# Kernel optimization log

Measured on AMD Instinct MI355X. Metric: run time of the kernel, lower is better.

Reference implementation:

```python
import jax, jax.numpy as jnp
import numpy as np

B, I, H, MS, M = 8192, 1024, 1024, 64, 16
TAU = 1.0


def setup_inputs() -> dict:
    key = jax.random.key(0)
    ks = jax.random.split(key, 24)
    s = 0.02
    eps = 1e-6
    return {
        "x": jax.random.normal(ks[0], (B, I), jnp.float32),
        "h": jax.random.normal(ks[1], (B, H), jnp.float32),
        "c": jax.random.normal(ks[2], (B, H), jnp.float32),
        "memory": jax.random.normal(ks[3], (B, M, MS), jnp.float32),
        "u_gs": jax.random.uniform(ks[4], (B, M), jnp.float32, eps, 1.0 - eps),
        "u_a": jax.random.uniform(ks[5], (B, 1), jnp.float32, eps, 1.0 - eps),
        "u_b": jax.random.uniform(ks[6], (B, 1), jnp.float32, eps, 1.0 - eps),
        # pre-concatenated gate weights, matching torch.cat((W_x2*, W_h2*, W_c2*), 0)
        "W_i": jax.random.normal(ks[7], (I + 2 * H, H), jnp.float32) * s,
        "b_i": jnp.zeros((H,), jnp.float32),
        "W_f": jax.random.normal(ks[8], (I + 2 * H, H), jnp.float32) * s,
        "b_f": jnp.ones((H,), jnp.float32),
        "W_o": jax.random.normal(ks[9], (I + 2 * H, H), jnp.float32) * s,
        "b_o": jnp.zeros((H,), jnp.float32),
        "W_cand": jax.random.normal(ks[10], (I + H, H), jnp.float32) * s,
        "b_cand": jnp.zeros((H,), jnp.float32),
        "W_m": jax.random.normal(ks[11], (H, MS), jnp.float32) * s,
        "b_m": jnp.zeros((MS,), jnp.float32),
        "w_a_h": jax.random.normal(ks[12], (H, 1), jnp.float32) * s,
        "w_a_x": jax.random.normal(ks[13], (I, 1), jnp.float32) * s,
        "w_a_r": jax.random.normal(ks[14], (MS, 1), jnp.float32) * s,
        "w_b_h": jax.random.normal(ks[15], (H, 1), jnp.float32) * s,
        "w_b_x": jax.random.normal(ks[16], (I, 1), jnp.float32) * s,
        "w_b_r": jax.random.normal(ks[17], (MS, 1), jnp.float32) * s,
    }


def reference(x, h, c, memory, u_gs, u_a, u_b,
              W_i, b_i, W_f, b_f, W_o, b_o, W_cand, b_cand,
              W_m, b_m, w_a_h, w_a_x, w_a_r, w_b_h, w_b_x, w_b_r):
    # LSTM-style gates with peephole c in the concatenated input
    xhc = jnp.concatenate([x, h, c], axis=1)            # [B, I+2H]
    i = jax.nn.sigmoid(xhc @ W_i + b_i)
    f = jax.nn.sigmoid(xhc @ W_f + b_f)
    cp = jnp.tanh(jnp.concatenate([x, h], axis=1) @ W_cand + b_cand)
    c_new = f * c + i * cp
    o = jax.nn.sigmoid(jnp.concatenate([x, h, c_new], axis=1) @ W_o + b_o)
    h_new = o * jnp.tanh(c_new)

    # memory-slot attention with Gumbel-softmax sampling
    micro = h_new @ W_m + b_m                           # [B, MS]
    logits = jnp.einsum('bmk,bk->bm', memory, micro)    # [B, M]
    g = -jnp.log(-jnp.log(u_gs))                        # Gumbel(0,1)
    attn = jax.nn.softmax((logits + g) / TAU, axis=-1)  # sampled_locations
    sampled = jnp.einsum('bmk,bm->bk', memory, attn) + 1.0  # [B, MS]

    # gumbel-sigmoid (binary concrete) for alpha / beta
    la = jnp.log(u_a) - jnp.log1p(-u_a)
    lb = jnp.log(u_b) - jnp.log1p(-u_b)
    alpha = jax.nn.sigmoid((h_new @ w_a_h + x @ w_a_x + sampled @ w_a_r + la) / TAU)
    beta = jax.nn.sigmoid((h_new @ w_b_h + x @ w_b_x + sampled @ w_b_r + lb) / TAU)

    # [B, 2H+2]
    return jnp.concatenate([h_new, c_new, alpha, beta], axis=1)
```

## Files before the change

kernel.cpp:

```cpp
#include <hip/hip_runtime.h>

typedef __bf16 bfrag __attribute__((ext_vector_type(8)));
typedef float f32x4 __attribute__((ext_vector_type(4)));

#define GLDS16(g, l) __builtin_amdgcn_global_load_lds( \
    (__attribute__((address_space(1))) void*)(g),      \
    (__attribute__((address_space(3))) void*)(l), 16, 0, 0)

__device__ __forceinline__ float bf2f(ushort u) {
    return __uint_as_float(((unsigned)u) << 16);
}
__device__ __forceinline__ ushort f2bf(float f) {
    unsigned u = __float_as_uint(f);
    u += 0x7fff + ((u >> 16) & 1);
    return (ushort)(u >> 16);
}
__device__ __forceinline__ float sigmoidf_(float v) {
    return 1.0f / (1.0f + expf(-v));
}

__global__ __launch_bounds__(256) void k_castcat(const float* __restrict__ x,
                                                 const float* __restrict__ h,
                                                 const float* __restrict__ c,
                                                 ushort* __restrict__ xhcb) {
    int idx = blockIdx.x * 256 + threadIdx.x;
    int row = idx / 384;
    int c8 = (idx - row * 384) * 8;
    const float* s = (c8 < 1024) ? &x[(size_t)row * 1024 + c8]
                   : (c8 < 2048) ? &h[(size_t)row * 1024 + (c8 - 1024)]
                                 : &c[(size_t)row * 1024 + (c8 - 2048)];
    float4 a = *(const float4*)s;
    float4 b = *(const float4*)(s + 4);
    ushort tmp[8] = {f2bf(a.x), f2bf(a.y), f2bf(a.z), f2bf(a.w),
                     f2bf(b.x), f2bf(b.y), f2bf(b.z), f2bf(b.w)};
    *(uint4*)&xhcb[(size_t)idx * 8] = *(uint4*)tmp;
}

struct TD { const float* src; ushort* dst; int src_ld; int dst_ld; int ktiles; int off; };
struct TA { TD d[6]; };

__global__ __launch_bounds__(256) void k_transAll(TA a) {
    __shared__ float tile[64][65];
    int bid = blockIdx.x;
    int ri = 0;
#pragma unroll
    for (int i = 1; i < 6; ++i) ri = (bid >= a.d[i].off) ? i : ri;
    const float* src = a.d[ri].src;
    ushort* dst = a.d[ri].dst;
    int src_ld = a.d[ri].src_ld, dst_ld = a.d[ri].dst_ld;
    int local = bid - a.d[ri].off;
    int bx = local % a.d[ri].ktiles;
    int by = local / a.d[ri].ktiles;
    int k0 = bx * 64, n0 = by * 64;
    int t = threadIdx.x;
    int c4 = (t & 15) * 4;
    int r = t >> 4;
#pragma unroll
    for (int i = 0; i < 4; ++i) {
        int rr = r + i * 16;
        float4 v = *(const float4*)&src[(size_t)(k0 + rr) * src_ld + n0 + c4];
        tile[rr][c4 + 0] = v.x; tile[rr][c4 + 1] = v.y;
        tile[rr][c4 + 2] = v.z; tile[rr][c4 + 3] = v.w;
    }
    __syncthreads();
    int kk8 = (t & 7) * 8;
    int nn = t >> 3;
#pragma unroll
    for (int i = 0; i < 2; ++i) {
        int n = nn + i * 32;
        ushort tmp[8];
#pragma unroll
        for (int j = 0; j < 8; ++j) tmp[j] = f2bf(tile[kk8 + j][n]);
        *(uint4*)&dst[(size_t)(n0 + n) * dst_ld + k0 + kk8] = *(uint4*)tmp;
    }
}

__global__ void k_biasf(const float* bi, const float* bf_, const float* bc,
                        const float* bo, float* dst) {
    int t = blockIdx.x * 256 + threadIdx.x;
    int g = t >> 10, n = t & 1023;
    const float* s = (g == 0) ? bi : (g == 1) ? bf_ : (g == 2) ? bc : bo;
    dst[t] = s[n];
}

__global__ __launch_bounds__(256) void k_gemm1(const ushort* __restrict__ xhcb,
                                               const ushort* __restrict__ WT,
                                               const float* __restrict__ bias,
                                               ushort* __restrict__ Pre) {
    __shared__ __align__(16) ushort As[128 * 32];
    __shared__ __align__(16) ushort Bs[128 * 32];
    int t = threadIdx.x;
    int m0 = blockIdx.x * 128, n0 = blockIdx.y * 128;
    int Kext = (n0 >= 2048) ? 2048 : 3072;
    int w = t >> 6, l = t & 63;
    int wm = (w & 1) * 64, wn = (w >> 1) * 64;
    int lane16 = l & 15, quad = l >> 4;
    int sr = t >> 2;
    int sko = (((t & 3) ^ ((sr >> 1) & 3))) * 8;
    int sw8 = ((lane16 >> 1) & 3) * 8;
    f32x4 acc[4][4] = {};

    for (int k0 = 0; k0 < Kext; k0 += 32) {
        GLDS16(xhcb + (size_t)(m0 + sr) * 3072 + k0 + sko,       As + t * 8);
        GLDS16(xhcb + (size_t)(m0 + sr + 64) * 3072 + k0 + sko,  As + 2048 + t * 8);
        GLDS16(WT + (size_t)(n0 + sr) * 3072 + k0 + sko,         Bs + t * 8);
        GLDS16(WT + (size_t)(n0 + sr + 64) * 3072 + k0 + sko,    Bs + 2048 + t * 8);
        __syncthreads();
        bfrag af[4], bfr[4];
#pragma unroll
        for (int i = 0; i < 4; ++i) {
            af[i]  = *(const bfrag*)&As[(wm + i * 16 + lane16) * 32 + ((quad * 8) ^ sw8)];
            bfr[i] = *(const bfrag*)&Bs[(wn + i * 16 + lane16) * 32 + ((quad * 8) ^ sw8)];
        }
#pragma unroll
        for (int i = 0; i < 4; ++i)
#pragma unroll
            for (int j = 0; j < 4; ++j)
                acc[i][j] = __builtin_amdgcn_mfma_f32_16x16x32_bf16(af[i], bfr[j], acc[i][j], 0, 0, 0);
        __syncthreads();
    }
#pragma unroll
    for (int i = 0; i < 4; ++i) {
#pragma unroll
        for (int j = 0; j < 4; ++j) {
            int col = n0 + wn + j * 16 + lane16;
            float bv = bias[col];
            int rbase = m0 + wm + i * 16 + quad * 4;
#pragma unroll
            for (int r = 0; r < 4; ++r)
                Pre[(size_t)(rbase + r) * 4096 + col] = f2bf(acc[i][j][r] + bv);
        }
    }
}

__global__ __launch_bounds__(256) void k_cnew(const ushort* __restrict__ Pre,
                                              const float* __restrict__ cin,
                                              ushort* __restrict__ Cnewb,
                                              float* __restrict__ out) {
    int idx8 = blockIdx.x * 256 + threadIdx.x;
    int b = idx8 >> 7;
    int n8 = (idx8 & 127) * 8;
    uint4 vi = *(const uint4*)(Pre + (size_t)b * 4096 + n8);
    uint4 vf = *(const uint4*)(Pre + (size_t)b * 4096 + 1024 + n8);
    uint4 vc = *(const uint4*)(Pre + (size_t)b * 4096 + 2048 + n8);
    float4 c0 = *(const float4*)(cin + (size_t)b * 1024 + n8);
    float4 c1 = *(const float4*)(cin + (size_t)b * 1024 + n8 + 4);
    const ushort* pi = (const ushort*)&vi;
    const ushort* pf = (const ushort*)&vf;
    const ushort* pc = (const ushort*)&vc;
    float cv[8] = {c0.x, c0.y, c0.z, c0.w, c1.x, c1.y, c1.z, c1.w};
    float cn[8];
    ushort cb[8];
#pragma unroll
    for (int j = 0; j < 8; ++j) {
        float iv = sigmoidf_(bf2f(pi[j]));
        float fv = sigmoidf_(bf2f(pf[j]));
        float cp = tanhf(bf2f(pc[j]));
        cn[j] = fv * cv[j] + iv * cp;
        cb[j] = f2bf(cn[j]);
    }
    *(uint4*)(Cnewb + (size_t)b * 1024 + n8) = *(uint4*)cb;
    float* orow = out + (size_t)b * 2050 + 1024 + n8;
#pragma unroll
    for (int j = 0; j < 4; ++j)
        *(float2*)(orow + j * 2) = make_float2(cn[j * 2], cn[j * 2 + 1]);
}

__global__ __launch_bounds__(256) void k_gemm2(const ushort* __restrict__ Cnewb,
                                               const ushort* __restrict__ WoCT,
                                               const ushort* __restrict__ Pre,
                                               ushort* __restrict__ Hnewb,
                                               float* __restrict__ out) {
    __shared__ __align__(16) ushort As[128 * 32];
    __shared__ __align__(16) ushort Bs[128 * 32];
    int t = threadIdx.x;
    int m0 = blockIdx.x * 128, n0 = blockIdx.y * 128;
    int w = t >> 6, l = t & 63;
    int wm = (w & 1) * 64, wn = (w >> 1) * 64;
    int lane16 = l & 15, quad = l >> 4;
    int sr = t >> 2;
    int sko = (((t & 3) ^ ((sr >> 1) & 3))) * 8;
    int sw8 = ((lane16 >> 1) & 3) * 8;
    f32x4 acc[4][4] = {};

    for (int k0 = 0; k0 < 1024; k0 += 32) {
        GLDS16(Cnewb + (size_t)(m0 + sr) * 1024 + k0 + sko,       As + t * 8);
        GLDS16(Cnewb + (size_t)(m0 + sr + 64) * 1024 + k0 + sko,  As + 2048 + t * 8);
        GLDS16(WoCT + (size_t)(n0 + sr) * 1024 + k0 + sko,        Bs + t * 8);
        GLDS16(WoCT + (size_t)(n0 + sr + 64) * 1024 + k0 + sko,   Bs + 2048 + t * 8);
        __syncthreads();
        bfrag af[4], bfr[4];
#pragma unroll
        for (int i = 0; i < 4; ++i) {
            af[i]  = *(const bfrag*)&As[(wm + i * 16 + lane16) * 32 + ((quad * 8) ^ sw8)];
            bfr[i] = *(const bfrag*)&Bs[(wn + i * 16 + lane16) * 32 + ((quad * 8) ^ sw8)];
        }
#pragma unroll
        for (int i = 0; i < 4; ++i)
#pragma unroll
            for (int j = 0; j < 4; ++j)
                acc[i][j] = __builtin_amdgcn_mfma_f32_16x16x32_bf16(af[i], bfr[j], acc[i][j], 0, 0, 0);
        __syncthreads();
    }
#pragma unroll
    for (int i = 0; i < 4; ++i) {
#pragma unroll
        for (int j = 0; j < 4; ++j) {
            int col = n0 + wn + j * 16 + lane16;
            int rbase = m0 + wm + i * 16 + quad * 4;
#pragma unroll
            for (int r = 0; r < 4; ++r) {
                int row = rbase + r;
                float opre = acc[i][j][r] + bf2f(Pre[(size_t)row * 4096 + 3072 + col]);
                float o = sigmoidf_(opre);
                float cnv = bf2f(Cnewb[(size_t)row * 1024 + col]);
                float hv = o * tanhf(cnv);
                Hnewb[(size_t)row * 1024 + col] = f2bf(hv);
                out[(size_t)row * 2050 + col] = hv;
            }
        }
    }
}

__global__ __launch_bounds__(256) void k_attn(
    const ushort* __restrict__ Hnewb, const float* __restrict__ outr,
    const float* __restrict__ x, const float* __restrict__ memory,
    const float* __restrict__ u_gs, const float* __restrict__ u_a,
    const float* __restrict__ u_b, const ushort* __restrict__ WmT,
    const float* __restrict__ b_m,
    const float* __restrict__ w_a_h, const float* __restrict__ w_a_x,
    const float* __restrict__ w_a_r, const float* __restrict__ w_b_h,
    const float* __restrict__ w_b_x, const float* __restrict__ w_b_r,
    float* __restrict__ out) {
    __shared__ float sMicro[16 * 64];
    __shared__ float sAttn[16 * 16];
    __shared__ float sSamp[16 * 64];

    int b0 = blockIdx.x * 16;
    int t = threadIdx.x;
    int w = t >> 6, l = t & 63;
    int lane16 = l & 15, quad = l >> 4;

    {
        f32x4 acc = {0.f, 0.f, 0.f, 0.f};
        const ushort* Ab = Hnewb + (size_t)(b0 + lane16) * 1024 + quad * 8;
        const ushort* Bb = WmT + (size_t)(w * 16 + lane16) * 1024 + quad * 8;
#pragma unroll 4
        for (int k0 = 0; k0 < 1024; k0 += 32) {
            bfrag av = *(const bfrag*)(Ab + k0);
            bfrag bv = *(const bfrag*)(Bb + k0);
            acc = __builtin_amdgcn_mfma_f32_16x16x32_bf16(av, bv, acc, 0, 0, 0);
        }
        float bm = b_m[w * 16 + lane16];
#pragma unroll
        for (int r = 0; r < 4; ++r)
            sMicro[(quad * 4 + r) * 64 + w * 16 + lane16] = acc[r] + bm;
    }
    __syncthreads();

    {
        int r = t >> 4, m = t & 15;
        const float4* mem4 = (const float4*)(memory + (size_t)(b0 + r) * 1024 + m * 64);
        float lg = 0.f;
#pragma unroll
        for (int k4 = 0; k4 < 16; ++k4) {
            float4 mv = mem4[k4];
            const float* sm = &sMicro[r * 64 + k4 * 4];
            lg += mv.x * sm[0] + mv.y * sm[1] + mv.z * sm[2] + mv.w * sm[3];
        }
        float u = u_gs[(b0 + r) * 16 + m];
        float z = lg - logf(-logf(u));
        float zm = z;
        for (int off = 8; off; off >>= 1) zm = fmaxf(zm, __shfl_xor(zm, off, 16));
        float p = expf(z - zm);
        float ps = p;
        for (int off = 8; off; off >>= 1) ps += __shfl_xor(ps, off, 16);
        sAttn[r * 16 + m] = p / ps;
    }
    __syncthreads();

#pragma unroll
    for (int q = 0; q < 4; ++q) {
        int r = w * 4 + q;
        const float* mem = memory + (size_t)(b0 + r) * 1024 + l;
        float s = 0.f;
#pragma unroll
        for (int m = 0; m < 16; ++m) s += sAttn[r * 16 + m] * mem[m * 64];
        sSamp[r * 64 + l] = s + 1.0f;
    }
    __syncthreads();

    {
        int r = t >> 4, s16 = t & 15;
        size_t hoff = (size_t)(b0 + r) * 2050;
        size_t xoff = (size_t)(b0 + r) * 1024;
        float za = 0.f, zb = 0.f;
        for (int kk = 0; kk < 64; ++kk) {
            int k = s16 + kk * 16;
            float hv = outr[hoff + k];
            float xv = x[xoff + k];
            za += hv * w_a_h[k] + xv * w_a_x[k];
            zb += hv * w_b_h[k] + xv * w_b_x[k];
        }
#pragma unroll
        for (int k = s16 * 4; k < s16 * 4 + 4; ++k) {
            float sv = sSamp[r * 64 + k];
            za += sv * w_a_r[k];
            zb += sv * w_b_r[k];
        }
        for (int off = 8; off; off >>= 1) {
            za += __shfl_xor(za, off, 16);
            zb += __shfl_xor(zb, off, 16);
        }
        if (s16 == 0) {
            float ua = u_a[b0 + r];
            float ub = u_b[b0 + r];
            float la = logf(ua) - log1pf(-ua);
            float lb = logf(ub) - log1pf(-ub);
            out[(size_t)(b0 + r) * 2050 + 2048] = sigmoidf_(za + la);
            out[(size_t)(b0 + r) * 2050 + 2049] = sigmoidf_(zb + lb);
        }
    }
}

extern "C" void kernel_launch(void* const* d_in, const int* in_sizes, int n_in,
                              void* d_out, int out_size, void* d_ws, size_t ws_size,
                              hipStream_t stream) {
    const float* x      = (const float*)d_in[0];
    const float* h      = (const float*)d_in[1];
    const float* c      = (const float*)d_in[2];
    const float* memory = (const float*)d_in[3];
    const float* u_gs   = (const float*)d_in[4];
    const float* u_a    = (const float*)d_in[5];
    const float* u_b    = (const float*)d_in[6];
    const float* W_i    = (const float*)d_in[7];
    const float* b_i    = (const float*)d_in[8];
    const float* W_f    = (const float*)d_in[9];
    const float* b_f    = (const float*)d_in[10];
    const float* W_o    = (const float*)d_in[11];
    const float* b_o    = (const float*)d_in[12];
    const float* W_cand = (const float*)d_in[13];
    const float* b_cand = (const float*)d_in[14];
    const float* W_m    = (const float*)d_in[15];
    const float* b_m    = (const float*)d_in[16];
    const float* w_a_h  = (const float*)d_in[17];
    const float* w_a_x  = (const float*)d_in[18];
    const float* w_a_r  = (const float*)d_in[19];
    const float* w_b_h  = (const float*)d_in[20];
    const float* w_b_x  = (const float*)d_in[21];
    const float* w_b_r  = (const float*)d_in[22];
    float* out = (float*)d_out;

    char* ws = (char*)d_ws;
    ushort* WT    = (ushort*)(ws);
    ushort* WoCT  = (ushort*)(ws + 25165824);
    ushort* Pre   = (ushort*)(ws + 27262976);
    ushort* xhcb  = (ushort*)(ws + 94371840);
    float*  Biasf = (float*)(ws + 144703488);
    ushort* WmT   = (ushort*)(ws + 144719872);
    ushort* Cnewb = xhcb;
    ushort* Hnewb = WT;

    k_castcat<<<12288, 256, 0, stream>>>(x, h, c, xhcb);

    TA ta;
    ta.d[0] = {W_i,                      WT,                        1024, 3072, 48, 0};
    ta.d[1] = {W_f,                      WT + (size_t)1024 * 3072,  1024, 3072, 48, 768};
    ta.d[2] = {W_cand,                   WT + (size_t)2048 * 3072,  1024, 3072, 32, 1536};
    ta.d[3] = {W_o,                      WT + (size_t)3072 * 3072,  1024, 3072, 48, 2048};
    ta.d[4] = {W_o + (size_t)2048 * 1024, WoCT,                     1024, 1024, 16, 2816};
    ta.d[5] = {W_m,                      WmT,                         64, 1024, 16, 3072};
    k_transAll<<<3088, 256, 0, stream>>>(ta);
    k_biasf<<<16, 256, 0, stream>>>(b_i, b_f, b_cand, b_o, Biasf);

    k_gemm1<<<dim3(64, 32), 256, 0, stream>>>(xhcb, WT, Biasf, Pre);
    k_cnew<<<4096, 256, 0, stream>>>(Pre, c, Cnewb, out);
    k_gemm2<<<dim3(64, 8), 256, 0, stream>>>(Cnewb, WoCT, Pre, Hnewb, out);
    k_attn<<<512, 256, 0, stream>>>(Hnewb, out, x, memory, u_gs, u_a, u_b, WmT, b_m,
                                    w_a_h, w_a_x, w_a_r, w_b_h, w_b_x, w_b_r, out);
}
```

Baseline: 572.0 us.

## Double GEMM K-tile to 64, fuse prep kernels, split gemm1 by K length

Both GEMM kernels now stage 64-wide K slices in LDS instead of 32, with a new XOR swizzle. This halves the number of barrier-separated iterations and doubles the MFMA work per sync. The cast/concat, weight transpose and bias-copy kernels are merged into one launch. It also stops transposing the unused last K-block of W_o for the fused gate GEMM. gemm1 is split into two templated launches with compile-time K (3072 and 2048), removing the runtime K branch. The cost is twice the LDS per block, which may reduce occupancy.

```diff
diff --git a/kernel.cpp b/kernel.cpp
--- a/kernel.cpp
+++ b/kernel.cpp
@@ -19,104 +19,116 @@
     return 1.0f / (1.0f + expf(-v));
 }
 
-__global__ __launch_bounds__(256) void k_castcat(const float* __restrict__ x,
-                                                 const float* __restrict__ h,
-                                                 const float* __restrict__ c,
-                                                 ushort* __restrict__ xhcb) {
-    int idx = blockIdx.x * 256 + threadIdx.x;
-    int row = idx / 384;
-    int c8 = (idx - row * 384) * 8;
-    const float* s = (c8 < 1024) ? &x[(size_t)row * 1024 + c8]
-                   : (c8 < 2048) ? &h[(size_t)row * 1024 + (c8 - 1024)]
-                                 : &c[(size_t)row * 1024 + (c8 - 2048)];
-    float4 a = *(const float4*)s;
-    float4 b = *(const float4*)(s + 4);
-    ushort tmp[8] = {f2bf(a.x), f2bf(a.y), f2bf(a.z), f2bf(a.w),
-                     f2bf(b.x), f2bf(b.y), f2bf(b.z), f2bf(b.w)};
-    *(uint4*)&xhcb[(size_t)idx * 8] = *(uint4*)tmp;
-}
-
 struct TD { const float* src; ushort* dst; int src_ld; int dst_ld; int ktiles; int off; };
 struct TA { TD d[6]; };
 
-__global__ __launch_bounds__(256) void k_transAll(TA a) {
+__global__ __launch_bounds__(256) void k_prep(const float* __restrict__ x,
+                                              const float* __restrict__ h,
+                                              const float* __restrict__ c,
+                                              ushort* __restrict__ xhcb, TA a,
+                                              const float* __restrict__ bi,
+                                              const float* __restrict__ bf_,
+                                              const float* __restrict__ bc,
+                                              const float* __restrict__ bo,
+                                              float* __restrict__ Biasf) {
     __shared__ float tile[64][65];
     int bid = blockIdx.x;
-    int ri = 0;
-#pragma unroll
-    for (int i = 1; i < 6; ++i) ri = (bid >= a.d[i].off) ? i : ri;
-    const float* src = a.d[ri].src;
-    ushort* dst = a.d[ri].dst;
-    int src_ld = a.d[ri].src_ld, dst_ld = a.d[ri].dst_ld;
-    int local = bid - a.d[ri].off;
-    int bx = local % a.d[ri].ktiles;
-    int by = local / a.d[ri].ktiles;
-    int k0 = bx * 64, n0 = by * 64;
     int t = threadIdx.x;
-    int c4 = (t & 15) * 4;
-    int r = t >> 4;
-#pragma unroll
-    for (int i = 0; i < 4; ++i) {
-        int rr = r + i * 16;
-        float4 v = *(const float4*)&src[(size_t)(k0 + rr) * src_ld + n0 + c4];
-        tile[rr][c4 + 0] = v.x; tile[rr][c4 + 1] = v.y;
-        tile[rr][c4 + 2] = v.z; tile[rr][c4 + 3] = v.w;
-    }
-    __syncthreads();
-    int kk8 = (t & 7) * 8;
-    int nn = t >> 3;
-#pragma unroll
-    for (int i = 0; i < 2; ++i) {
-        int n = nn + i * 32;
-        ushort tmp[8];
-#pragma unroll
-        for (int j = 0; j < 8; ++j) tmp[j] = f2bf(tile[kk8 + j][n]);
-        *(uint4*)&dst[(size_t)(n0 + n) * dst_ld + k0 + kk8] = *(uint4*)tmp;
-    }
-}
-
-__global__ void k_biasf(const float* bi, const float* bf_, const float* bc,
-                        const float* bo, float* dst) {
-    int t = blockIdx.x * 256 + threadIdx.x;
-    int g = t >> 10, n = t & 1023;
-    const float* s = (g == 0) ? bi : (g == 1) ? bf_ : (g == 2) ? bc : bo;
-    dst[t] = s[n];
-}
-
-__global__ __launch_bounds__(256) void k_gemm1(const ushort* __restrict__ xhcb,
-                                               const ushort* __restrict__ WT,
-                                               const float* __restrict__ bias,
-                                               ushort* __restrict__ Pre) {
-    __shared__ __align__(16) ushort As[128 * 32];
-    __shared__ __align__(16) ushort Bs[128 * 32];
+    if (bid < 12288) {
+        int idx = bid * 256 + t;
+        int row = idx / 384;
+        int c8 = (idx - row * 384) * 8;
+        const float* s = (c8 < 1024) ? &x[(size_t)row * 1024 + c8]
+                       : (c8 < 2048) ? &h[(size_t)row * 1024 + (c8 - 1024)]
+                                     : &c[(size_t)row * 1024 + (c8 - 2048)];
+        float4 va = *(const float4*)s;
+        float4 vb = *(const float4*)(s + 4);
+        ushort tmp[8] = {f2bf(va.x), f2bf(va.y), f2bf(va.z), f2bf(va.w),
+                         f2bf(vb.x), f2bf(vb.y), f2bf(vb.z), f2bf(vb.w)};
+        *(uint4*)&xhcb[(size_t)idx * 8] = *(uint4*)tmp;
+    } else if (bid < 15120) {
+        int tb = bid - 12288;
+        int ri = 0;
+#pragma unroll
+        for (int i = 1; i < 6; ++i) ri = (tb >= a.d[i].off) ? i : ri;
+        const float* src = a.d[ri].src;
+        ushort* dst = a.d[ri].dst;
+        int src_ld = a.d[ri].src_ld, dst_ld = a.d[ri].dst_ld;
+        int local = tb - a.d[ri].off;
+        int bx = local % a.d[ri].ktiles;
+        int by = local / a.d[ri].ktiles;
+        int k0 = bx * 64, n0 = by * 64;
+        int c4 = (t & 15) * 4;
+        int r = t >> 4;
+#pragma unroll
+        for (int i = 0; i < 4; ++i) {
+            int rr = r + i * 16;
+            float4 v = *(const float4*)&src[(size_t)(k0 + rr) * src_ld + n0 + c4];
+            tile[rr][c4 + 0] = v.x; tile[rr][c4 + 1] = v.y;
+            tile[rr][c4 + 2] = v.z; tile[rr][c4 + 3] = v.w;
+        }
+        __syncthreads();
+        int kk8 = (t & 7) * 8;
+        int nn = t >> 3;
+#pragma unroll
+        for (int i = 0; i < 2; ++i) {
+            int n = nn + i * 32;
+            ushort tmp[8];
+#pragma unroll
+            for (int j = 0; j < 8; ++j) tmp[j] = f2bf(tile[kk8 + j][n]);
+            *(uint4*)&dst[(size_t)(n0 + n) * dst_ld + k0 + kk8] = *(uint4*)tmp;
+        }
+    } else {
+        int idx = (bid - 15120) * 256 + t;
+        int g = idx >> 10, n = idx & 1023;
+        const float* s = (g == 0) ? bi : (g == 1) ? bf_ : (g == 2) ? bc : bo;
+        Biasf[idx] = s[n];
+    }
+}
+
+template <int KTOT>
+__global__ __launch_bounds__(256) void k_gemm1t(const ushort* __restrict__ xhcb,
+                                                const ushort* __restrict__ WT,
+                                                const float* __restrict__ bias,
+                                                ushort* __restrict__ Pre, int nbase) {
+    __shared__ __align__(16) ushort As[128 * 64];
+    __shared__ __align__(16) ushort Bs[128 * 64];
     int t = threadIdx.x;
-    int m0 = blockIdx.x * 128, n0 = blockIdx.y * 128;
-    int Kext = (n0 >= 2048) ? 2048 : 3072;
+    int m0 = blockIdx.x * 128, n0 = nbase + blockIdx.y * 128;
     int w = t >> 6, l = t & 63;
     int wm = (w & 1) * 64, wn = (w >> 1) * 64;
     int lane16 = l & 15, quad = l >> 4;
-    int sr = t >> 2;
-    int sko = (((t & 3) ^ ((sr >> 1) & 3))) * 8;
-    int sw8 = ((lane16 >> 1) & 3) * 8;
+    int rowt = t >> 3;
+    int kg = (t & 7) ^ (rowt & 7);
+    int r7 = lane16 & 7;
     f32x4 acc[4][4] = {};
 
-    for (int k0 = 0; k0 < Kext; k0 += 32) {
-        GLDS16(xhcb + (size_t)(m0 + sr) * 3072 + k0 + sko,       As + t * 8);
-        GLDS16(xhcb + (size_t)(m0 + sr + 64) * 3072 + k0 + sko,  As + 2048 + t * 8);
-        GLDS16(WT + (size_t)(n0 + sr) * 3072 + k0 + sko,         Bs + t * 8);
-        GLDS16(WT + (size_t)(n0 + sr + 64) * 3072 + k0 + sko,    Bs + 2048 + t * 8);
+    const ushort* Abase = xhcb + (size_t)(m0 + rowt) * 3072 + kg * 8;
+    const ushort* Bbase = WT + (size_t)(n0 + rowt) * 3072 + kg * 8;
+
+    for (int k0 = 0; k0 < KTOT; k0 += 64) {
+#pragma unroll
+        for (int q = 0; q < 4; ++q)
+            GLDS16(Abase + (size_t)q * 32 * 3072 + k0, As + q * 2048 + t * 8);
+#pragma unroll
+        for (int q = 0; q < 4; ++q)
+            GLDS16(Bbase + (size_t)q * 32 * 3072 + k0, Bs + q * 2048 + t * 8);
         __syncthreads();
-        bfrag af[4], bfr[4];
-#pragma unroll
-        for (int i = 0; i < 4; ++i) {
-            af[i]  = *(const bfrag*)&As[(wm + i * 16 + lane16) * 32 + ((quad * 8) ^ sw8)];
-            bfr[i] = *(const bfrag*)&Bs[(wn + i * 16 + lane16) * 32 + ((quad * 8) ^ sw8)];
-        }
-#pragma unroll
-        for (int i = 0; i < 4; ++i)
-#pragma unroll
-            for (int j = 0; j < 4; ++j)
-                acc[i][j] = __builtin_amdgcn_mfma_f32_16x16x32_bf16(af[i], bfr[j], acc[i][j], 0, 0, 0);
+#pragma unroll
+        for (int hh = 0; hh < 2; ++hh) {
+            int slot8 = ((hh * 4 + quad) ^ r7) * 8;
+            bfrag af[4], bfr[4];
+#pragma unroll
+            for (int i = 0; i < 4; ++i) {
+                af[i]  = *(const bfrag*)&As[(wm + i * 16 + lane16) * 64 + slot8];
+                bfr[i] = *(const bfrag*)&Bs[(wn + i * 16 + lane16) * 64 + slot8];
+            }
+#pragma unroll
+            for (int i = 0; i < 4; ++i)
+#pragma unroll
+                for (int j = 0; j < 4; ++j)
+                    acc[i][j] = __builtin_amdgcn_mfma_f32_16x16x32_bf16(af[i], bfr[j], acc[i][j], 0, 0, 0);
+        }
         __syncthreads();
     }
 #pragma unroll
@@ -171,35 +183,44 @@
                                                const ushort* __restrict__ Pre,
                                                ushort* __restrict__ Hnewb,
                                                float* __restrict__ out) {
-    __shared__ __align__(16) ushort As[128 * 32];
-    __shared__ __align__(16) ushort Bs[128 * 32];
+    __shared__ __align__(16) ushort As[128 * 64];
+    __shared__ __align__(16) ushort Bs[128 * 64];
     int t = threadIdx.x;
     int m0 = blockIdx.x * 128, n0 = blockIdx.y * 128;
     int w = t >> 6, l = t & 63;
     int wm = (w & 1) * 64, wn = (w >> 1) * 64;
     int lane16 = l & 15, quad = l >> 4;
-    int sr = t >> 2;
-    int sko = (((t & 3) ^ ((sr >> 1) & 3))) * 8;
-    int sw8 = ((lane16 >> 1) & 3) * 8;
+    int rowt = t >> 3;
+    int kg = (t & 7) ^ (rowt & 7);
+    int r7 = lane16 & 7;
     f32x4 acc[4][4] = {};
 
-    for (int k0 = 0; k0 < 1024; k0 += 32) {
-        GLDS16(Cnewb + (size_t)(m0 + sr) * 1024 + k0 + sko,       As + t * 8);
-        GLDS16(Cnewb + (size_t)(m0 + sr + 64) * 1024 + k0 + sko,  As + 2048 + t * 8);
-        GLDS16(WoCT + (size_t)(n0 + sr) * 1024 + k0 + sko,        Bs + t * 8);
-        GLDS16(WoCT + (size_t)(n0 + sr + 64) * 1024 + k0 + sko,   Bs + 2048 + t * 8);
+    const ushort* Abase = Cnewb + (size_t)(m0 + rowt) * 1024 + kg * 8;
+    const ushort* Bbase = WoCT + (size_t)(n0 + rowt) * 1024 + kg * 8;
+
+    for (int k0 = 0; k0 < 1024; k0 += 64) {
+#pragma unroll
+        for (int q = 0; q < 4; ++q)
+            GLDS16(Abase + (size_t)q * 32 * 1024 + k0, As + q * 2048 + t * 8);
+#pragma unroll
+        for (int q = 0; q < 4; ++q)
+            GLDS16(Bbase + (size_t)q * 32 * 1024 + k0, Bs + q * 2048 + t * 8);
         __syncthreads();
-        bfrag af[4], bfr[4];
-#pragma unroll
-        for (int i = 0; i < 4; ++i) {
-            af[i]  = *(const bfrag*)&As[(wm + i * 16 + lane16) * 32 + ((quad * 8) ^ sw8)];
-            bfr[i] = *(const bfrag*)&Bs[(wn + i * 16 + lane16) * 32 + ((quad * 8) ^ sw8)];
-        }
-#pragma unroll
-        for (int i = 0; i < 4; ++i)
-#pragma unroll
-            for (int j = 0; j < 4; ++j)
-                acc[i][j] = __builtin_amdgcn_mfma_f32_16x16x32_bf16(af[i], bfr[j], acc[i][j], 0, 0, 0);
+#pragma unroll
+        for (int hh = 0; hh < 2; ++hh) {
+            int slot8 = ((hh * 4 + quad) ^ r7) * 8;
+            bfrag af[4], bfr[4];
+#pragma unroll
+            for (int i = 0; i < 4; ++i) {
+                af[i]  = *(const bfrag*)&As[(wm + i * 16 + lane16) * 64 + slot8];
+                bfr[i] = *(const bfrag*)&Bs[(wn + i * 16 + lane16) * 64 + slot8];
+            }
+#pragma unroll
+            for (int i = 0; i < 4; ++i)
+#pragma unroll
+                for (int j = 0; j < 4; ++j)
+                    acc[i][j] = __builtin_amdgcn_mfma_f32_16x16x32_bf16(af[i], bfr[j], acc[i][j], 0, 0, 0);
+        }
         __syncthreads();
     }
 #pragma unroll
@@ -361,19 +382,18 @@
     ushort* Cnewb = xhcb;
     ushort* Hnewb = WT;
 
-    k_castcat<<<12288, 256, 0, stream>>>(x, h, c, xhcb);
-
     TA ta;
-    ta.d[0] = {W_i,                      WT,                        1024, 3072, 48, 0};
-    ta.d[1] = {W_f,                      WT + (size_t)1024 * 3072,  1024, 3072, 48, 768};
-    ta.d[2] = {W_cand,                   WT + (size_t)2048 * 3072,  1024, 3072, 32, 1536};
-    ta.d[3] = {W_o,                      WT + (size_t)3072 * 3072,  1024, 3072, 48, 2048};
-    ta.d[4] = {W_o + (size_t)2048 * 1024, WoCT,                     1024, 1024, 16, 2816};
-    ta.d[5] = {W_m,                      WmT,                         64, 1024, 16, 3072};
-    k_transAll<<<3088, 256, 0, stream>>>(ta);
-    k_biasf<<<16, 256, 0, stream>>>(b_i, b_f, b_cand, b_o, Biasf);
-
-    k_gemm1<<<dim3(64, 32), 256, 0, stream>>>(xhcb, WT, Biasf, Pre);
+    ta.d[0] = {W_i,                       WT,                        1024, 3072, 48, 0};
+    ta.d[1] = {W_f,                       WT + (size_t)1024 * 3072,  1024, 3072, 48, 768};
+    ta.d[2] = {W_cand,                    WT + (size_t)2048 * 3072,  1024, 3072, 32, 1536};
+    ta.d[3] = {W_o,                       WT + (size_t)3072 * 3072,  1024, 3072, 32, 2048};
+    ta.d[4] = {W_o + (size_t)2048 * 1024, WoCT,                      1024, 1024, 16, 2560};
+    ta.d[5] = {W_m,                       WmT,                         64, 1024, 16, 2816};
+
+    k_prep<<<15136, 256, 0, stream>>>(x, h, c, xhcb, ta, b_i, b_f, b_cand, b_o, Biasf);
+
+    k_gemm1t<3072><<<dim3(64, 16), 256, 0, stream>>>(xhcb, WT, Biasf, Pre, 0);
+    k_gemm1t<2048><<<dim3(64, 16), 256, 0, stream>>>(xhcb, WT, Biasf, Pre, 2048);
     k_cnew<<<4096, 256, 0, stream>>>(Pre, c, Cnewb, out);
     k_gemm2<<<dim3(64, 8), 256, 0, stream>>>(Cnewb, WoCT, Pre, Hnewb, out);
     k_attn<<<512, 256, 0, stream>>>(Hnewb, out, x, memory, u_gs, u_a, u_b, WmT, b_m,
```

After: 515.9 us. -9.8%, faster.
